# Kernel optimization log

Hardware: AMD Instinct MI355X
Metric: run time of the kernel (lower is better)

The kernel has to match this reference:

```python
import jax, jax.numpy as jnp
import numpy as np

M = 4  # mixture size of the AttentionStem value embedding

def unfold_windows(a, kh, kw, Hout, Wout):
    # a: [..., Hp, Wp] -> [..., Hout, Wout, kh, kw] (stride-1 sliding windows, cropped)
    rows = []
    for i in range(kh):
        cols = [a[..., i:i + Hout, j:j + Wout] for j in range(kw)]
        rows.append(jnp.stack(cols, axis=-1))
    return jnp.stack(rows, axis=-2)

def attention_stem(x, qw, kw_, vw, emb_a, emb_b, emb_mix, kh, kw, pad):
    # x: [B,Cin,H,W]; qw/kw_: [Cin,Co]; vw: [M,Cin,Co]; emb_a:[Co,kh]; emb_b:[Co,kw]; emb_mix:[M,Co]
    B, Cin, H, W = x.shape
    pl, pr, pt, pb = pad  # F.pad order (left,right,top,bottom)
    xp = jnp.pad(x, ((0, 0), (0, 0), (pt, pb), (pl, pr)))
    Hp, Wp = xp.shape[2], xp.shape[3]
    Hout = min(Hp - kh + 1, H)
    Wout = min(Wp - kw + 1, W)
    q = jnp.einsum('bchw,co->bohw', x[:, :, :Hout, :Wout], qw)       # 1x1 conv query
    k = jnp.einsum('bchw,co->bohw', xp, kw_)                          # 1x1 conv key on padded
    v = jnp.einsum('bchw,mco->mbohw', xp, vw)                         # m 1x1 conv values
    k_win = unfold_windows(k, kh, kw, Hout, Wout)                     # [B,Co,Ho,Wo,kh,kw]
    v_win = unfold_windows(v, kh, kw, Hout, Wout)                     # [M,B,Co,Ho,Wo,kh,kw]
    # mixture relative-position embedding, softmax over mixtures per (kh,kw) offset
    la = emb_mix @ emb_a                                              # [M,kh]
    lb = emb_mix @ emb_b                                              # [M,kw]
    emb = jax.nn.softmax(la[:, :, None] + lb[:, None, :], axis=0)     # [M,kh,kw]
    v_agg = jnp.einsum('mkl,mbohwkl->bohwkl', emb, v_win)             # [B,Co,Ho,Wo,kh,kw]
    K = kh * kw
    scores = jnp.einsum('bohw,bohwkl->bhwkl', q, k_win).reshape(B, Hout, Wout, K)
    attn = jax.nn.softmax(scores, axis=-1).reshape(B, Hout, Wout, kh, kw)
    out = jnp.einsum('bhwkl,bohwkl->bohw', attn, v_agg)               # [B,Co,Ho,Wo]
    return out

def bn_relu(x, g, b):
    # training-mode BatchNorm2d + ReLU
    mu = x.mean(axis=(0, 2, 3), keepdims=True)
    var = x.var(axis=(0, 2, 3), keepdims=True)
    y = (x - mu) * jax.lax.rsqrt(var + 1e-5) * g[None, :, None, None] + b[None, :, None, None]
    return jax.nn.relu(y)

def _params(key):
    ks = jax.random.split(key, 18)
    def w(k, shape):
        return jax.random.normal(k, shape, dtype=jnp.float32) * 0.1
    cfg = [(1, 64, 1, 5), (64, 128, 2, 5), (128, 16, 2, 5)]
    p = {}
    i = 0
    for s, (ci, co, kh, kw) in enumerate(cfg):
        p[f'p{s}_q'] = w(ks[i], (ci, co)); i += 1
        p[f'p{s}_k'] = w(ks[i], (ci, co)); i += 1
        p[f'p{s}_v'] = w(ks[i], (M, ci, co)); i += 1
        p[f'p{s}_ea'] = w(ks[i], (co, kh)); i += 1
        p[f'p{s}_eb'] = w(ks[i], (co, kw)); i += 1
        p[f'p{s}_em'] = w(ks[i], (M, co)); i += 1
        p[f'p{s}_g'] = jnp.ones((co,), jnp.float32)
        p[f'p{s}_b'] = jnp.zeros((co,), jnp.float32)
    return p

def setup_inputs() -> dict:
    key = jax.random.key(0)
    kx, kp = jax.random.split(key)
    inp = {'x': jax.random.normal(kx, (2, 1, 8, 3000), dtype=jnp.float32)}
    inp.update(_params(kp))
    return inp

def reference(x,
              p0_q, p0_k, p0_v, p0_ea, p0_eb, p0_em, p0_g, p0_b,
              p1_q, p1_k, p1_v, p1_ea, p1_eb, p1_em, p1_g, p1_b,
              p2_q, p2_k, p2_v, p2_ea, p2_eb, p2_em, p2_g, p2_b):
    h = attention_stem(x, p0_q, p0_k, p0_v, p0_ea, p0_eb, p0_em, 1, 5, (2, 2, 0, 0))
    h = bn_relu(h, p0_g, p0_b)[:, :, ::2, ::2]                        # MaxPool2d(1,2) == stride-2 subsample
    h = attention_stem(h, p1_q, p1_k, p1_v, p1_ea, p1_eb, p1_em, 2, 5, (2, 2, 1, 1))
    h = bn_relu(h, p1_g, p1_b)[:, :, ::2, ::2]
    h = attention_stem(h, p2_q, p2_k, p2_v, p2_ea, p2_eb, p2_em, 2, 5, (2, 2, 0, 0))
    h = bn_relu(h, p2_g, p2_b)
    B, C, H, W = h.shape
    nW = W // 56                                                       # AvgPool2d((1,56))
    return h[:, :, :, :nW * 56].reshape(B, C, H, nW, 56).mean(-1)
```

## Files before the change

kernel.cpp:

```cpp
#include <hip/hip_runtime.h>
#include <math.h>


#define TPB 256

__global__ void prep0_kernel(const float* __restrict__ ea,
                             const float* __restrict__ eb,
                             const float* __restrict__ em,
                             const float* __restrict__ qw,
                             const float* __restrict__ kw_,
                             const float* __restrict__ vw,
                             float* __restrict__ par) {
    const int M4 = 4, Co = 64, kw = 5;
    __shared__ float la[4];
    __shared__ float lb[20];
    __shared__ float embs[20];
    int tid = threadIdx.x;
    if (tid < 64) {
        float p = qw[tid] * kw_[tid];
#pragma unroll
        for (int d = 1; d < 64; d <<= 1) p += __shfl_xor(p, d, 64);
        if (tid == 0) par[0] = p;
    }
    if (tid >= 64 && tid < 64 + M4) {
        int m = tid - 64;
        float s = 0.f;
        for (int o = 0; o < Co; ++o) s += em[m * Co + o] * ea[o];
        la[m] = s;
    }
    if (tid >= 128 && tid < 128 + M4 * kw) {
        int r = tid - 128;
        int m = r / kw, l = r % kw;
        float s = 0.f;
        for (int o = 0; o < Co; ++o) s += em[m * Co + o] * eb[o * kw + l];
        lb[m * kw + l] = s;
    }
    __syncthreads();
    if (tid < 5) {
        float lg[4];
        float mx = -1e30f;
        for (int m = 0; m < M4; ++m) {
            lg[m] = la[m] + lb[m * kw + tid];
            mx = fmaxf(mx, lg[m]);
        }
        float sum = 0.f;
        for (int m = 0; m < M4; ++m) { lg[m] = expf(lg[m] - mx); sum += lg[m]; }
        float inv = 1.f / sum;
        for (int m = 0; m < M4; ++m) embs[tid * 4 + m] = lg[m] * inv;
    }
    __syncthreads();
    for (int e = tid; e < 5 * 64; e += blockDim.x) {
        int t = e / 64, o = e - t * 64;
        float s = 0.f;
        for (int m = 0; m < M4; ++m) s += embs[t * 4 + m] * vw[m * 64 + o];
        par[1 + e] = s;
    }
}

__global__ void attn_out0_kernel(const float* __restrict__ x,
                                 const float* __restrict__ par,
                                 float* __restrict__ h0raw,
                                 float2* __restrict__ part0) {
    __shared__ float wsh[5][256];
    __shared__ float vsh[5 * 64];
    __shared__ float wred[4][20];
    __shared__ float wfin[20];
    int tid = threadIdx.x;
    int b = blockIdx.y;
    int oz = blockIdx.z;
    int n0 = blockIdx.x * 256;
    int n = n0 + tid;
    for (int i = tid; i < 320; i += 256) vsh[i] = par[1 + i];
    float c0 = par[0];
    float warr[5];
    if (n < 24000) {
        int h = n / 3000, w = n - h * 3000;
        const float* xr = x + b * 24000 + h * 3000;
        float xc = xr[w];
        float xs[5], s[5];
#pragma unroll
        for (int t = 0; t < 5; ++t) {
            int col = w + t - 2;
            xs[t] = (col >= 0 && col < 3000) ? xr[col] : 0.f;
            s[t] = c0 * xc * xs[t];
        }
        float mx = s[0];
#pragma unroll
        for (int t = 1; t < 5; ++t) mx = fmaxf(mx, s[t]);
        float sum = 0.f;
#pragma unroll
        for (int t = 0; t < 5; ++t) { s[t] = expf(s[t] - mx); sum += s[t]; }
        float inv = 1.f / sum;
#pragma unroll
        for (int t = 0; t < 5; ++t) warr[t] = s[t] * inv * xs[t];
    } else {
#pragma unroll
        for (int t = 0; t < 5; ++t) warr[t] = 0.f;
    }
#pragma unroll
    for (int t = 0; t < 5; ++t) wsh[t][tid] = warr[t];
    float p[20];
#pragma unroll
    for (int t = 0; t < 5; ++t) p[t] = warr[t];
    {
        int k = 5;
#pragma unroll
        for (int t = 0; t < 5; ++t)
#pragma unroll
            for (int t2 = t; t2 < 5; ++t2) p[k++] = warr[t] * warr[t2];
    }
#pragma unroll
    for (int d = 1; d < 64; d <<= 1)
#pragma unroll
        for (int i = 0; i < 20; ++i) p[i] += __shfl_xor(p[i], d, 64);
    if ((tid & 63) == 0)
#pragma unroll
        for (int i = 0; i < 20; ++i) wred[tid >> 6][i] = p[i];
    __syncthreads();
    if (tid < 20)
        wfin[tid] = wred[0][tid] + wred[1][tid] + wred[2][tid] + wred[3][tid];
    __syncthreads();
    int jq = tid & 63, og = tid >> 6;
    int nq = n0 + jq * 4;
    int h = nq / 3000, w0 = nq - h * 3000;
    bool st = (nq < 24000) && ((h & 1) == 0);
    float wq[5][4];
#pragma unroll
    for (int t = 0; t < 5; ++t)
#pragma unroll
        for (int j = 0; j < 4; ++j) wq[t][j] = wsh[t][jq * 4 + j];
    int obase = oz * 32 + og * 8;
    for (int oi = 0; oi < 8; ++oi) {
        int o = obase + oi;
        float4 v = make_float4(0.f, 0.f, 0.f, 0.f);
#pragma unroll
        for (int t = 0; t < 5; ++t) {
            float vo = vsh[t * 64 + o];
            v.x = fmaf(wq[t][0], vo, v.x);
            v.y = fmaf(wq[t][1], vo, v.y);
            v.z = fmaf(wq[t][2], vo, v.z);
            v.w = fmaf(wq[t][3], vo, v.w);
        }
        if (st) {
            size_t base = ((size_t)b * 64 + o) * 6000 + (h >> 1) * 1500 + (w0 >> 1);
            *(float2*)&h0raw[base] = make_float2(v.x, v.z);
        }
    }
    if (tid < 32) {
        int o = oz * 32 + tid;
        float vt[5];
#pragma unroll
        for (int t = 0; t < 5; ++t) vt[t] = vsh[t * 64 + o];
        float s = 0.f, s2 = 0.f;
#pragma unroll
        for (int t = 0; t < 5; ++t) s = fmaf(vt[t], wfin[t], s);
        int k = 5;
#pragma unroll
        for (int t = 0; t < 5; ++t)
#pragma unroll
            for (int t2 = t; t2 < 5; ++t2) {
                float coef = (t == t2) ? vt[t] * vt[t] : 2.f * vt[t] * vt[t2];
                s2 = fmaf(coef, wfin[k], s2);
                ++k;
            }
        int chunk = b * gridDim.x + blockIdx.x;
        part0[(size_t)o * 188 + chunk] = make_float2(s, s2);
    }
}

__global__ void prep_stage1_kernel(const float* __restrict__ ea,
                                   const float* __restrict__ eb,
                                   const float* __restrict__ em,
                                   const float* __restrict__ qw,
                                   const float* __restrict__ kw_,
                                   const float* __restrict__ vw,
                                   float* __restrict__ Wqk,
                                   float* __restrict__ Av,
                                   const float2* __restrict__ part0,
                                   float* __restrict__ mr0) {
    const int M4 = 4, Co = 128, kh = 2, kw = 5, Cin = 64;
    __shared__ float la[8];
    __shared__ float lb[20];
    __shared__ float embs[40];
    int tid = threadIdx.x;
    if (blockIdx.x == 0 && tid < 64) {
        double s = 0.0, s2 = 0.0;
        for (int i = 0; i < 188; ++i) {
            float2 p = part0[(size_t)tid * 188 + i];
            s += p.x; s2 += p.y;
        }
        double mean = s / 48000.0;
        double var = s2 / 48000.0 - mean * mean;
        mr0[tid] = (float)mean;
        mr0[64 + tid] = (float)(1.0 / sqrt(var + 1e-5));
    }
    if (tid < M4 * kh) {
        int m = tid / kh, k = tid % kh;
        float s = 0.f;
        for (int o = 0; o < Co; ++o) s += em[m * Co + o] * ea[o * kh + k];
        la[tid] = s;
    }
    if (tid >= 64 && tid < 64 + M4 * kw) {
        int r = tid - 64;
        int m = r / kw, l = r % kw;
        float s = 0.f;
        for (int o = 0; o < Co; ++o) s += em[m * Co + o] * eb[o * kw + l];
        lb[r] = s;
    }
    __syncthreads();
    if (tid < 10) {
        int k = tid / kw, l = tid % kw;
        float lg[4];
        float mx = -1e30f;
        for (int m = 0; m < M4; ++m) {
            lg[m] = la[m * kh + k] + lb[m * kw + l];
            mx = fmaxf(mx, lg[m]);
        }
        float sum = 0.f;
        for (int m = 0; m < M4; ++m) { lg[m] = expf(lg[m] - mx); sum += lg[m]; }
        float inv = 1.f / sum;
        for (int m = 0; m < M4; ++m) embs[tid * 4 + m] = lg[m] * inv;
    }
    __syncthreads();
    const int TOT1 = 256 * 64;
    const int TOT2 = 640 * 128;
    for (int e = blockIdx.x * blockDim.x + tid; e < TOT1 + TOT2;
         e += gridDim.x * blockDim.x) {
        if (e < TOT1) {
            int m = e / Cin, c = e - m * Cin;
            Wqk[e] = (m < Co) ? qw[c * Co + m] : kw_[c * Co + (m - Co)];
        } else {
            int e2 = e - TOT1;
            int k = e2 / Co, o = e2 - k * Co;
            int c = k / 10, t = k - c * 10;
            float val = 0.f;
            for (int m = 0; m < M4; ++m)
                val += embs[t * 4 + m] * vw[(m * Cin + c) * Co + o];
            Av[e2] = val;
        }
    }
}

__global__ void prep_wcat_kernel(const float* __restrict__ ea,
                                 const float* __restrict__ eb,
                                 const float* __restrict__ em,
                                 const float* __restrict__ qw,
                                 const float* __restrict__ kw_,
                                 const float* __restrict__ vw,
                                 float* __restrict__ Wcat,
                                 int Co, int kh, int kw, int Cin,
                                 const float2* __restrict__ part,
                                 float* __restrict__ mr,
                                 int Cprev, int NCH, int count) {
    const int M4 = 4;
    __shared__ float la[8];
    __shared__ float lb[20];
    __shared__ float embs[40];
    int K = kh * kw;
    int tid = threadIdx.x;
    if (blockIdx.x == 0 && tid < Cprev) {
        double s = 0.0, s2 = 0.0;
        for (int i = 0; i < NCH; ++i) {
            float2 p = part[(size_t)tid * NCH + i];
            s += p.x; s2 += p.y;
        }
        double mean = s / count;
        double var = s2 / count - mean * mean;
        mr[tid] = (float)mean;
        mr[Cprev + tid] = (float)(1.0 / sqrt(var + 1e-5));
    }
    if (tid < M4 * kh) {
        int m = tid / kh, k = tid % kh;
        float s = 0.f;
        for (int o = 0; o < Co; ++o) s += em[m * Co + o] * ea[o * kh + k];
        la[tid] = s;
    }
    if (tid >= 64 && tid < 64 + M4 * kw) {
        int r = tid - 64;
        int m = r / kw, l = r % kw;
        float s = 0.f;
        for (int o = 0; o < Co; ++o) s += em[m * Co + o] * eb[o * kw + l];
        lb[r] = s;
    }
    __syncthreads();
    if (tid < K) {
        int k = tid / kw, l = tid % kw;
        float lg[4];
        float mx = -1e30f;
        for (int m = 0; m < M4; ++m) {
            lg[m] = la[m * kh + k] + lb[m * kw + l];
            mx = fmaxf(mx, lg[m]);
        }
        float sum = 0.f;
        for (int m = 0; m < M4; ++m) { lg[m] = expf(lg[m] - mx); sum += lg[m]; }
        float inv = 1.f / sum;
        for (int m = 0; m < M4; ++m) embs[tid * 4 + m] = lg[m] * inv;
    }
    __syncthreads();
    int Mtot = (2 + K) * Co;
    long long total = (long long)Mtot * Cin;
    for (long long e = (long long)blockIdx.x * blockDim.x + tid; e < total;
         e += (long long)gridDim.x * blockDim.x) {
        int m = (int)(e / Cin);
        int c = (int)(e - (long long)m * Cin);
        float val;
        if (m < Co) {
            val = qw[c * Co + m];
        } else if (m < 2 * Co) {
            val = kw_[c * Co + (m - Co)];
        } else {
            int mz = m - 2 * Co;
            int t = mz / Co;
            int o = mz - t * Co;
            val = 0.f;
            for (int mm = 0; mm < M4; ++mm)
                val += embs[t * 4 + mm] * vw[(mm * Cin + c) * Co + o];
        }
        Wcat[e] = val;
    }
}

__launch_bounds__(256, 4)
__global__ void gemm_qkbn_kernel(const float* __restrict__ A,
                                 const float* __restrict__ xraw,
                                 const float* __restrict__ mr,
                                 const float* __restrict__ g,
                                 const float* __restrict__ bb,
                                 float* __restrict__ qk,
                                 float* __restrict__ z,
                                 int M, int N, int K, int twoCo) {
    __shared__ float As[32][132];
    __shared__ float Bs[32][132];
    __shared__ float scale[128], shift[128];
    int tid = threadIdx.x;
    int b = blockIdx.z;
    int m0 = blockIdx.y * 128, n0 = blockIdx.x * 128;
    int Mz = M - twoCo;
    float acc[8][8] = {{0.f}};
    int am = tid >> 1, ak = (tid & 1) * 16;
    int bk = tid >> 3, bn = (tid & 7) * 16;
    int tm = tid & 15, tn = tid >> 4;
    for (int c = tid; c < K; c += 256) {
        float sc = mr[K + c] * g[c];
        scale[c] = sc;
        shift[c] = bb[c] - mr[c] * sc;
    }
    __syncthreads();

    for (int k0 = 0; k0 < K; k0 += 32) {
        {
            int mA = m0 + am;
            const float* Ap = A + (size_t)mA * K + k0 + ak;
#pragma unroll
            for (int q = 0; q < 4; ++q) {
                float4 v = (mA < M) ? *(const float4*)(Ap + q * 4)
                                    : make_float4(0.f, 0.f, 0.f, 0.f);
                int kk = ak + q * 4;
                As[kk + 0][am] = v.x;
                As[kk + 1][am] = v.y;
                As[kk + 2][am] = v.z;
                As[kk + 3][am] = v.w;
            }
        }
        {
            int c = k0 + bk;
            float sc = scale[c], sf = shift[c];
            const float* Xp = xraw + ((size_t)b * K + c) * N + n0 + bn;
            if (n0 + 128 <= N) {
#pragma unroll
                for (int q = 0; q < 4; ++q) {
                    float4 v = *(const float4*)(Xp + q * 4);
                    v.x = fmaxf(fmaf(v.x, sc, sf), 0.f);
                    v.y = fmaxf(fmaf(v.y, sc, sf), 0.f);
                    v.z = fmaxf(fmaf(v.z, sc, sf), 0.f);
                    v.w = fmaxf(fmaf(v.w, sc, sf), 0.f);
                    *(float4*)&Bs[bk][bn + q * 4] = v;
                }
            } else {
#pragma unroll
                for (int q = 0; q < 16; ++q) {
                    int n = n0 + bn + q;
                    Bs[bk][bn + q] = (n < N) ? fmaxf(fmaf(Xp[q], sc, sf), 0.f) : 0.f;
                }
            }
        }
        __syncthreads();
#pragma unroll 8
        for (int k = 0; k < 32; ++k) {
            float4 a0 = *(const float4*)&As[k][tm * 4];
            float4 a1 = *(const float4*)&As[k][64 + tm * 4];
            float4 b0 = *(const float4*)&Bs[k][tn * 4];
            float4 b1 = *(const float4*)&Bs[k][64 + tn * 4];
            float av[8] = {a0.x, a0.y, a0.z, a0.w, a1.x, a1.y, a1.z, a1.w};
            float bv[8] = {b0.x, b0.y, b0.z, b0.w, b1.x, b1.y, b1.z, b1.w};
#pragma unroll
            for (int i = 0; i < 8; ++i)
#pragma unroll
                for (int j = 0; j < 8; ++j)
                    acc[i][j] = fmaf(av[i], bv[j], acc[i][j]);
        }
        __syncthreads();
    }
    bool fullN = (n0 + 128 <= N);
#pragma unroll
    for (int iq = 0; iq < 2; ++iq) {
        int mb = m0 + iq * 64 + tm * 4;
        if (mb >= M) continue;
        if (mb < twoCo) {
#pragma unroll
            for (int jq = 0; jq < 2; ++jq)
#pragma unroll
                for (int jj = 0; jj < 4; ++jj) {
                    int n = n0 + jq * 64 + tn * 4 + jj;
                    if (n < N) {
                        float4 v = make_float4(acc[iq * 4 + 0][jq * 4 + jj],
                                               acc[iq * 4 + 1][jq * 4 + jj],
                                               acc[iq * 4 + 2][jq * 4 + jj],
                                               acc[iq * 4 + 3][jq * 4 + jj]);
                        *(float4*)&qk[((size_t)b * N + n) * twoCo + mb] = v;
                    }
                }
        } else {
#pragma unroll
            for (int i = 0; i < 4; ++i) {
                int row = mb + i - twoCo;
                float* zp = &z[((size_t)b * Mz + row) * N];
#pragma unroll
                for (int jq = 0; jq < 2; ++jq) {
                    int nb_ = n0 + jq * 64 + tn * 4;
                    if (fullN) {
                        *(float4*)&zp[nb_] = make_float4(acc[iq * 4 + i][jq * 4 + 0],
                                                         acc[iq * 4 + i][jq * 4 + 1],
                                                         acc[iq * 4 + i][jq * 4 + 2],
                                                         acc[iq * 4 + i][jq * 4 + 3]);
                    } else {
#pragma unroll
                        for (int jj = 0; jj < 4; ++jj)
                            if (nb_ + jj < N) zp[nb_ + jj] = acc[iq * 4 + i][jq * 4 + jj];
                    }
                }
            }
        }
    }
}

template <int KH, int KW, int CO, int NPB>
__global__ void attn_v3_kernel(const float* __restrict__ qk,
                               float* __restrict__ attn,
                               int H, int W, int Ho, int Wo, int pt, int pl) {
    const int K = KH * KW;
    __shared__ float ssh[NPB][K];
    int tid = threadIdx.x;
    int b = blockIdx.y;
    int ln = tid / K, t = tid - ln * K;
    int Nout = Ho * Wo;
    int n = blockIdx.x * NPB + ln;
    bool active = (tid < NPB * K) && (n < Nout);
    int HWin = H * W;
    float sv = 0.f;
    if (active) {
        int ho = n / Wo, wo = n - ho * Wo;
        int row = ho + t / KW - pt, col = wo + t % KW - pl;
        if (row >= 0 && row < H && col >= 0 && col < W) {
            const float* qp = qk + ((size_t)b * HWin + ho * W + wo) * (2 * CO);
            const float* kp = qk + ((size_t)b * HWin + (size_t)row * W + col) * (2 * CO) + CO;
#pragma unroll
            for (int o = 0; o < CO; o += 4) {
                float4 q4 = *(const float4*)(qp + o);
                float4 k4 = *(const float4*)(kp + o);
                sv += q4.x * k4.x + q4.y * k4.y + q4.z * k4.z + q4.w * k4.w;
            }
        }
        ssh[ln][t] = sv;
    }
    __syncthreads();
    if (active) {
        float mx = ssh[ln][0];
#pragma unroll
        for (int tt = 1; tt < K; ++tt) mx = fmaxf(mx, ssh[ln][tt]);
        float sum = 0.f;
#pragma unroll
        for (int tt = 0; tt < K; ++tt) sum += expf(ssh[ln][tt] - mx);
        float num = expf(sv - mx);
        attn[((size_t)b * K + t) * Nout + n] = num / sum;
    }
}

template <int KH, int KW, int SK>
__launch_bounds__(256)
__global__ void vgemm_kernel(const float* __restrict__ Av,
                             const float* __restrict__ xraw,
                             const float* __restrict__ attn,
                             const float* __restrict__ mr,
                             const float* __restrict__ g,
                             const float* __restrict__ bb,
                             float* __restrict__ partial,
                             int Cin, int Co,
                             int H, int W, int Ho, int Wo,
                             int pt, int pl) {
    const int KK = KH * KW;
    const int BK = 4 * KK;
    __shared__ float As[BK][68];
    __shared__ float Bs[BK][68];
    __shared__ float scale[128], shift[128];
    __shared__ float attn_s[KK][64];
    __shared__ int ho_s[64], wo_s[64];
    int tid = threadIdx.x;
    int b = blockIdx.z;
    int mt = blockIdx.y / SK, sk = blockIdx.y % SK;
    int m0 = mt * 64;
    int n0 = blockIdx.x * 64;
    int Nin = H * W, Nout = Ho * Wo;
    int Cpb = Cin / SK;
    int c_base = sk * Cpb;
    int Klocal = Cpb * KK;
    for (int c = tid; c < Cin; c += 256) {
        float sc = mr[Cin + c] * g[c];
        scale[c] = sc;
        shift[c] = bb[c] - mr[c] * sc;
    }
    for (int e = tid; e < KK * 64; e += 256) {
        int t = e >> 6, j = e & 63;
        int n = n0 + j;
        attn_s[t][j] = (n < Nout) ? attn[((size_t)b * KK + t) * Nout + n] : 0.f;
    }
    if (tid < 64) {
        int n = n0 + tid;
        ho_s[tid] = n / Wo;
        wo_s[tid] = n % Wo;
    }
    __syncthreads();
    float acc[4][4] = {{0.f}};
    int tm = tid & 15, tn = tid >> 4;
    for (int k0 = 0; k0 < Klocal; k0 += BK) {
#pragma unroll
        for (int it = 0; it < 10; ++it) {
            int e = it * 256 + tid;
            int kk = e >> 6, mm = e & 63;
            As[kk][mm] = Av[(size_t)(c_base * KK + k0 + kk) * Co + m0 + mm];
        }
#pragma unroll
        for (int it = 0; it < 10; ++it) {
            int e = it * 256 + tid;
            int kk = e >> 6, j = e & 63;
            int kg = k0 + kk;
            int cc = c_base + kg / KK, t = kg % KK;
            int dk = t / KW, dl = t % KW;
            int row = ho_s[j] + dk - pt;
            int col = wo_s[j] + dl - pl;
            float v = 0.f;
            if ((n0 + j) < Nout && row >= 0 && row < H && col >= 0 && col < W) {
                float xv = xraw[((size_t)b * Cin + cc) * Nin + row * W + col];
                xv = fmaxf(fmaf(xv, scale[cc], shift[cc]), 0.f);
                v = xv * attn_s[t][j];
            }
            Bs[kk][j] = v;
        }
        __syncthreads();
#pragma unroll 8
        for (int k = 0; k < BK; ++k) {
            float4 a4 = *(const float4*)&As[k][tm * 4];
            float4 b4 = *(const float4*)&Bs[k][tn * 4];
            float av[4] = {a4.x, a4.y, a4.z, a4.w};
            float bv[4] = {b4.x, b4.y, b4.z, b4.w};
#pragma unroll
            for (int i = 0; i < 4; ++i)
#pragma unroll
                for (int j = 0; j < 4; ++j)
                    acc[i][j] = fmaf(av[i], bv[j], acc[i][j]);
        }
        __syncthreads();
    }
    int B = gridDim.z;
#pragma unroll
    for (int i = 0; i < 4; ++i) {
        int o = m0 + tm * 4 + i;
        float* pp = &partial[(((size_t)sk * B + b) * Co + o) * Nout];
        int n = n0 + tn * 4;
        if (n + 3 < Nout) {
            *(float4*)&pp[n] = make_float4(acc[i][0], acc[i][1], acc[i][2], acc[i][3]);
        } else {
#pragma unroll
            for (int j = 0; j < 4; ++j)
                if (n + j < Nout) pp[n + j] = acc[i][j];
        }
    }
}

__global__ void vreduce_kernel(const float* __restrict__ partial,
                               float* __restrict__ h1raw,
                               float2* __restrict__ part1) {
    int tid = threadIdx.x;
    int by = blockIdx.y;
    int b = by >> 7, o = by & 127;
    int n = blockIdx.x * 1024 + tid * 4;
    float4 v = make_float4(0.f, 0.f, 0.f, 0.f);
    if (n < 6000) {
#pragma unroll
        for (int sk = 0; sk < 4; ++sk) {
            float4 p = *(const float4*)&partial[(((size_t)sk * 2 + b) * 128 + o) * 6000 + n];
            v.x += p.x; v.y += p.y; v.z += p.z; v.w += p.w;
        }
        int ho = n / 1500, wo = n - ho * 1500;
        if ((ho & 1) == 0) {
            size_t base = ((size_t)b * 128 + o) * 1500 + (ho >> 1) * 750 + (wo >> 1);
            *(float2*)&h1raw[base] = make_float2(v.x, v.z);
        }
    }
    float s = v.x + v.y + v.z + v.w;
    float s2 = v.x * v.x + v.y * v.y + v.z * v.z + v.w * v.w;
    __shared__ float sh[TPB], sh2[TPB];
    sh[tid] = s; sh2[tid] = s2;
    __syncthreads();
    for (int st = TPB / 2; st > 0; st >>= 1) {
        if (tid < st) { sh[tid] += sh[tid + st]; sh2[tid] += sh2[tid + st]; }
        __syncthreads();
    }
    if (tid == 0)
        part1[(size_t)o * 12 + b * 6 + blockIdx.x] = make_float2(sh[0], sh2[0]);
}

template <int KH, int KW>
__global__ void combine_stats_kernel(const float* __restrict__ z,
                                     const float* __restrict__ attn,
                                     float* __restrict__ out,
                                     float2* __restrict__ part,
                                     int Co, int Mz,
                                     int H, int W, int Ho, int Wo,
                                     int pt, int pl) {
    const int K = KH * KW;
    int tid = threadIdx.x;
    int bc = blockIdx.y;
    int b = bc / Co, o = bc - b * Co;
    int Nout = Ho * Wo, Nin = H * W;
    int n = blockIdx.x * blockDim.x + tid;
    float val = 0.f;
    if (n < Nout) {
        int ho = n / Wo, wo = n - ho * Wo;
#pragma unroll
        for (int dk = 0; dk < KH; ++dk) {
            int row = ho + dk - pt;
            if (row < 0 || row >= H) continue;
#pragma unroll
            for (int dl = 0; dl < KW; ++dl) {
                int col = wo + dl - pl;
                if (col < 0 || col >= W) continue;
                int t = dk * KW + dl;
                float a = attn[((size_t)b * K + t) * Nout + n];
                float zv = z[((size_t)b * Mz + t * Co + o) * Nin + row * W + col];
                val = fmaf(a, zv, val);
            }
        }
        out[((size_t)b * Co + o) * Nout + n] = val;
    }
    __shared__ float sh[TPB], sh2[TPB];
    sh[tid] = (n < Nout) ? val : 0.f;
    sh2[tid] = (n < Nout) ? val * val : 0.f;
    __syncthreads();
    for (int st = TPB / 2; st > 0; st >>= 1) {
        if (tid < st) { sh[tid] += sh[tid + st]; sh2[tid] += sh2[tid + st]; }
        __syncthreads();
    }
    if (tid == 0) {
        int chunk = b * gridDim.x + blockIdx.x;
        part[(size_t)o * (2 * gridDim.x) + chunk] = make_float2(sh[0], sh2[0]);
    }
}

__global__ void bn_avg_final_kernel(const float* __restrict__ x,
                                    const float2* __restrict__ part,
                                    const float* __restrict__ g,
                                    const float* __restrict__ bb,
                                    float* __restrict__ out,
                                    int B, int C, int W, int nW, int NCH) {
    int idx = blockIdx.x * blockDim.x + threadIdx.x;
    int N = B * C * nW;
    if (idx >= N) return;
    int j = idx % nW; int r = idx / nW;
    int c = r % C; int b = r / C;
    double s = 0.0, s2 = 0.0;
    for (int i = 0; i < NCH; ++i) {
        float2 p = part[(size_t)c * NCH + i];
        s += p.x; s2 += p.y;
    }
    double cnt = (double)B * W;
    double mean = s / cnt;
    double var = s2 / cnt - mean * mean;
    float rstd = (float)(1.0 / sqrt(var + 1e-5));
    float meanf = (float)mean, gg = g[c], bo = bb[c];
    const float* xb = x + ((long long)b * C + c) * W + j * 56;
    float acc = 0.f;
    for (int i = 0; i < 56; ++i) {
        float yn = (xb[i] - meanf) * rstd * gg + bo;
        acc += fmaxf(yn, 0.f);
    }
    out[idx] = acc * (1.f / 56.f);
}

extern "C" void kernel_launch(void* const* d_in, const int* in_sizes, int n_in,
                              void* d_out, int out_size, void* d_ws, size_t ws_size,
                              hipStream_t stream) {
    const float* x   = (const float*)d_in[0];
    const float* qw0 = (const float*)d_in[1];
    const float* kw0 = (const float*)d_in[2];
    const float* vw0 = (const float*)d_in[3];
    const float* ea0 = (const float*)d_in[4];
    const float* eb0 = (const float*)d_in[5];
    const float* em0 = (const float*)d_in[6];
    const float* g0  = (const float*)d_in[7];
    const float* b0  = (const float*)d_in[8];
    const float* qw1 = (const float*)d_in[9];
    const float* kw1 = (const float*)d_in[10];
    const float* vw1 = (const float*)d_in[11];
    const float* ea1 = (const float*)d_in[12];
    const float* eb1 = (const float*)d_in[13];
    const float* em1 = (const float*)d_in[14];
    const float* g1  = (const float*)d_in[15];
    const float* b1  = (const float*)d_in[16];
    const float* qw2 = (const float*)d_in[17];
    const float* kw2 = (const float*)d_in[18];
    const float* vw2 = (const float*)d_in[19];
    const float* ea2 = (const float*)d_in[20];
    const float* eb2 = (const float*)d_in[21];
    const float* em2 = (const float*)d_in[22];
    const float* g2  = (const float*)d_in[23];
    const float* b2  = (const float*)d_in[24];
    float* outp = (float*)d_out;
    (void)ws_size; (void)in_sizes; (void)n_in; (void)out_size;

    float* ws = (float*)d_ws;
    size_t off = 0;
    auto alloc = [&](size_t n) { float* p = ws + off; off += (n + 63) & ~(size_t)63; return p; };

    float* par0   = alloc(321);
    float* part0  = alloc(64 * 188 * 2);
    float* mr0    = alloc(128);
    float* h0raw  = alloc(2 * 64 * 6000);
    float* Wqk1   = alloc(256 * 64);
    float* Av1    = alloc(640 * 128);
    float* qk1    = alloc(2 * 6000 * 256);
    float* attn1  = alloc(2 * 10 * 6000);
    float* vpart  = alloc(4 * 2 * 128 * 6000);
    float* part1  = alloc(128 * 12 * 2);
    float* mr1    = alloc(256);
    float* h1raw  = alloc(2 * 128 * 1500);
    float* Wcat2  = alloc(192 * 128);
    float* qk2    = alloc(2 * 1500 * 32);
    float* z2     = alloc(2 * 160 * 1500);
    float* attn2  = alloc(2 * 10 * 750);
    float* part2  = alloc(16 * 6 * 2);
    float* s2     = alloc(2 * 16 * 750);

    auto grid = [](int n) { return (n + TPB - 1) / TPB; };

    prep0_kernel<<<1, TPB, 0, stream>>>(ea0, eb0, em0, qw0, kw0, vw0, par0);
    {
        dim3 g(94, 2, 2);
        attn_out0_kernel<<<g, TPB, 0, stream>>>(x, par0, h0raw, (float2*)part0);
    }
    prep_stage1_kernel<<<64, TPB, 0, stream>>>(ea1, eb1, em1, qw1, kw1, vw1,
        Wqk1, Av1, (const float2*)part0, mr0);
    {
        dim3 g(47, 2, 2);
        gemm_qkbn_kernel<<<g, TPB, 0, stream>>>(Wqk1, h0raw, mr0, g0, b0,
            qk1, qk1 , 256, 6000, 64, 256);
    }
    {
        dim3 g(6000 / 25, 2);
        attn_v3_kernel<2, 5, 128, 25><<<g, TPB, 0, stream>>>(qk1, attn1,
            4, 1500, 4, 1500, 1, 2);
    }
    {
        dim3 g(94, 2 * 4, 2);
        vgemm_kernel<2, 5, 4><<<g, TPB, 0, stream>>>(Av1, h0raw, attn1, mr0, g0, b0,
            vpart, 64, 128, 4, 1500, 4, 1500, 1, 2);
    }
    {
        dim3 g(6, 256);
        vreduce_kernel<<<g, TPB, 0, stream>>>(vpart, h1raw, (float2*)part1);
    }
    prep_wcat_kernel<<<24, TPB, 0, stream>>>(ea2, eb2, em2, qw2, kw2, vw2, Wcat2,
        16, 2, 5, 128, (const float2*)part1, mr1, 128, 12, 12000);
    {
        dim3 g(12, 2, 2);
        gemm_qkbn_kernel<<<g, TPB, 0, stream>>>(Wcat2, h1raw, mr1, g1, b1,
            qk2, z2, 192, 1500, 128, 32);
    }
    {
        dim3 g(750 / 25, 2);
        attn_v3_kernel<2, 5, 16, 25><<<g, TPB, 0, stream>>>(qk2, attn2,
            2, 750, 1, 750, 0, 2);
    }
    {
        dim3 g(3, 2 * 16);
        combine_stats_kernel<2, 5><<<g, TPB, 0, stream>>>(z2, attn2, s2,
            (float2*)part2, 16, 160, 2, 750, 1, 750, 0, 2);
    }
    bn_avg_final_kernel<<<grid(2 * 16 * 13), TPB, 0, stream>>>(s2, (const float2*)part2,
        g2, b2, outp, 2, 16, 750, 13, 6);
}
```

Measured before the change: 263.1 us.

## Fold q·k into Gram matrix and fuse stage-1 scores with softmax

Stage-1 attention scores are computed directly as x^T (Wq Wk^T) x using a precomputed 64x64 Gram matrix. This replaces the separate q/k GEMM that wrote a large qk buffer and the attention softmax pass, so both now run in one tiled kernel with a shared input window. The value GEMM is specialised to fixed shapes, stages the BN-ReLU input window and attention weights in shared memory, and halves the split-K factor, which shrinks the partial buffer and the reduction. In exchange each block does more serial work and the code is hardcoded to this layer's dimensions.

```diff
diff --git a/kernel.cpp b/kernel.cpp
--- a/kernel.cpp
+++ b/kernel.cpp
@@ -174,7 +174,7 @@
                                    const float* __restrict__ qw,
                                    const float* __restrict__ kw_,
                                    const float* __restrict__ vw,
-                                   float* __restrict__ Wqk,
+                                   float* __restrict__ G,
                                    float* __restrict__ Av,
                                    const float2* __restrict__ part0,
                                    float* __restrict__ mr0) {
@@ -222,15 +222,18 @@
         for (int m = 0; m < M4; ++m) embs[tid * 4 + m] = lg[m] * inv;
     }
     __syncthreads();
-    const int TOT1 = 256 * 64;
+    const int TOTG = 64 * 64;
     const int TOT2 = 640 * 128;
-    for (int e = blockIdx.x * blockDim.x + tid; e < TOT1 + TOT2;
-         e += gridDim.x * blockDim.x) {
-        if (e < TOT1) {
-            int m = e / Cin, c = e - m * Cin;
-            Wqk[e] = (m < Co) ? qw[c * Co + m] : kw_[c * Co + (m - Co)];
+    int nth = gridDim.x * blockDim.x;
+    for (int e = blockIdx.x * blockDim.x + tid; e < TOTG + TOT2; e += nth) {
+        if (e < TOTG) {
+            int c = e >> 6, c2 = e & 63;
+            float s = 0.f;
+            for (int o = 0; o < 128; ++o)
+                s = fmaf(qw[c * 128 + o], kw_[c2 * 128 + o], s);
+            G[e] = s;
         } else {
-            int e2 = e - TOT1;
+            int e2 = e - TOTG;
             int k = e2 / Co, o = e2 - k * Co;
             int c = k / 10, t = k - c * 10;
             float val = 0.f;
@@ -320,6 +323,216 @@
     }
 }
 
+__global__ void attn_v4_kernel(const float* __restrict__ G,
+                               const float* __restrict__ xraw,
+                               const float* __restrict__ mr,
+                               const float* __restrict__ g,
+                               const float* __restrict__ bb,
+                               float* __restrict__ attn) {
+    __shared__ float xw[64][2][68];
+    __shared__ float gbuf[64][64];
+    __shared__ float ssh[64][12];
+    __shared__ float scb[64], sfb[64];
+    int tid = threadIdx.x;
+    int chunk = blockIdx.x;
+    int ho = blockIdx.y;
+    int b = blockIdx.z;
+    int wo0 = chunk * 64;
+    if (tid < 64) {
+        float sc = mr[64 + tid] * g[tid];
+        scb[tid] = sc;
+        sfb[tid] = bb[tid] - mr[tid] * sc;
+    }
+    for (int e = tid; e < 4096; e += 256)
+        gbuf[e >> 6][e & 63] = G[e];
+    __syncthreads();
+    for (int e = tid; e < 64 * 136; e += 256) {
+        int c = e / 136;
+        int r2 = e - c * 136;
+        int r = r2 / 68, jj = r2 - r * 68;
+        int row = ho - 1 + r;
+        int col = wo0 + jj - 2;
+        float v = 0.f;
+        if (row >= 0 && col >= 0 && col < 1500) {
+            float xv = xraw[((size_t)b * 64 + c) * 6000 + row * 1500 + col];
+            v = fmaxf(fmaf(xv, scb[c], sfb[c]), 0.f);
+        }
+        xw[c][r][jj] = v;
+    }
+    __syncthreads();
+    int j = tid & 63, cg = tid >> 6;
+    float ul[16];
+#pragma unroll
+    for (int i = 0; i < 16; ++i) ul[i] = 0.f;
+    for (int c = 0; c < 64; ++c) {
+        float xv = xw[c][1][j + 2];
+#pragma unroll
+        for (int i = 0; i < 16; ++i)
+            ul[i] = fmaf(gbuf[c][cg * 16 + i], xv, ul[i]);
+    }
+    __syncthreads();
+#pragma unroll
+    for (int i = 0; i < 16; ++i) gbuf[cg * 16 + i][j] = ul[i];
+    __syncthreads();
+    int t0 = cg, t1 = cg + 4, t2 = cg + 8;
+    int dk0 = t0 / 5, dl0 = t0 % 5;
+    int dk1 = t1 / 5, dl1 = t1 % 5;
+    int dk2 = (t2 < 10) ? 1 : 0, dl2 = (t2 < 10) ? (t2 - 5) : 0;
+    float s0 = 0.f, s1 = 0.f, s2v = 0.f;
+    for (int c = 0; c < 64; ++c) {
+        float uv = gbuf[c][j];
+        s0 = fmaf(uv, xw[c][dk0][j + dl0], s0);
+        s1 = fmaf(uv, xw[c][dk1][j + dl1], s1);
+        if (t2 < 10) s2v = fmaf(uv, xw[c][dk2][j + dl2], s2v);
+    }
+    ssh[j][t0] = s0;
+    ssh[j][t1] = s1;
+    if (t2 < 10) ssh[j][t2] = s2v;
+    __syncthreads();
+    if (tid < 64 && wo0 + tid < 1500) {
+        float sc[10];
+        float mx = -1e30f;
+#pragma unroll
+        for (int t = 0; t < 10; ++t) { sc[t] = ssh[tid][t]; mx = fmaxf(mx, sc[t]); }
+        float sum = 0.f;
+#pragma unroll
+        for (int t = 0; t < 10; ++t) { sc[t] = expf(sc[t] - mx); sum += sc[t]; }
+        float inv = 1.f / sum;
+        int n = ho * 1500 + wo0 + tid;
+#pragma unroll
+        for (int t = 0; t < 10; ++t)
+            attn[((size_t)b * 10 + t) * 6000 + n] = sc[t] * inv;
+    }
+}
+
+__launch_bounds__(256)
+__global__ void vgemm_kernel(const float* __restrict__ Av,
+                             const float* __restrict__ xraw,
+                             const float* __restrict__ attn,
+                             const float* __restrict__ mr,
+                             const float* __restrict__ g,
+                             const float* __restrict__ bb,
+                             float* __restrict__ partial) {
+    __shared__ float As[40][68];
+    __shared__ float Bs[40][68];
+    __shared__ float xw[32][2][68];
+    __shared__ float att_s[10][64];
+    __shared__ float scl[32], sfl[32];
+    int tid = threadIdx.x;
+    int nt = blockIdx.x;
+    int ho = nt / 24, chunk = nt - ho * 24;
+    int wo0 = chunk * 64;
+    int my = blockIdx.y;
+    int mt = my >> 1, sk = my & 1;
+    int m0 = mt * 64;
+    int b = blockIdx.z;
+    int c_base = sk * 32;
+    if (tid < 32) {
+        int c = c_base + tid;
+        float sc = mr[64 + c] * g[c];
+        scl[tid] = sc;
+        sfl[tid] = bb[c] - mr[c] * sc;
+    }
+    __syncthreads();
+    for (int e = tid; e < 32 * 136; e += 256) {
+        int c = e / 136;
+        int r2 = e - c * 136;
+        int r = r2 / 68, jj = r2 - r * 68;
+        int row = ho - 1 + r;
+        int col = wo0 + jj - 2;
+        float v = 0.f;
+        if (row >= 0 && col >= 0 && col < 1500) {
+            float xv = xraw[((size_t)b * 64 + c_base + c) * 6000 + row * 1500 + col];
+            v = fmaxf(fmaf(xv, scl[c], sfl[c]), 0.f);
+        }
+        xw[c][r][jj] = v;
+    }
+    for (int e = tid; e < 640; e += 256) {
+        int t = e >> 6, jj = e & 63;
+        int col = wo0 + jj;
+        att_s[t][jj] = (col < 1500)
+            ? attn[((size_t)b * 10 + t) * 6000 + ho * 1500 + col] : 0.f;
+    }
+    __syncthreads();
+    float acc[4][4] = {{0.f}};
+    int tm = tid & 15, tn = tid >> 4;
+    int arow = c_base * 10;
+    for (int k0 = 0; k0 < 320; k0 += 40) {
+#pragma unroll
+        for (int it = 0; it < 10; ++it) {
+            int e = it * 256 + tid;
+            int kk = e >> 6, mm = e & 63;
+            As[kk][mm] = Av[(size_t)(arow + k0 + kk) * 128 + m0 + mm];
+        }
+#pragma unroll
+        for (int it = 0; it < 10; ++it) {
+            int e = it * 256 + tid;
+            int kk = e >> 6, jj = e & 63;
+            int kg = k0 + kk;
+            int cl = kg / 10, t = kg - cl * 10;
+            int dk = t / 5, dl = t - dk * 5;
+            Bs[kk][jj] = xw[cl][dk][jj + dl] * att_s[t][jj];
+        }
+        __syncthreads();
+#pragma unroll 8
+        for (int k = 0; k < 40; ++k) {
+            float4 a4 = *(const float4*)&As[k][tm * 4];
+            float4 b4 = *(const float4*)&Bs[k][tn * 4];
+            float av[4] = {a4.x, a4.y, a4.z, a4.w};
+            float bv[4] = {b4.x, b4.y, b4.z, b4.w};
+#pragma unroll
+            for (int i = 0; i < 4; ++i)
+#pragma unroll
+                for (int jx = 0; jx < 4; ++jx)
+                    acc[i][jx] = fmaf(av[i], bv[jx], acc[i][jx]);
+        }
+        __syncthreads();
+    }
+    int wo = wo0 + tn * 4;
+    if (wo < 1500) {
+        int n = ho * 1500 + wo;
+#pragma unroll
+        for (int i = 0; i < 4; ++i) {
+            int o = m0 + tm * 4 + i;
+            float* pp = &partial[(((size_t)sk * 2 + b) * 128 + o) * 6000 + n];
+            *(float4*)pp = make_float4(acc[i][0], acc[i][1], acc[i][2], acc[i][3]);
+        }
+    }
+}
+
+__global__ void vreduce_kernel(const float* __restrict__ partial,
+                               float* __restrict__ h1raw,
+                               float2* __restrict__ part1) {
+    int tid = threadIdx.x;
+    int by = blockIdx.y;
+    int b = by >> 7, o = by & 127;
+    int n = blockIdx.x * 1024 + tid * 4;
+    float4 v = make_float4(0.f, 0.f, 0.f, 0.f);
+    if (n < 6000) {
+#pragma unroll
+        for (int sk = 0; sk < 2; ++sk) {
+            float4 p = *(const float4*)&partial[(((size_t)sk * 2 + b) * 128 + o) * 6000 + n];
+            v.x += p.x; v.y += p.y; v.z += p.z; v.w += p.w;
+        }
+        int ho = n / 1500, wo = n - ho * 1500;
+        if ((ho & 1) == 0) {
+            size_t base = ((size_t)b * 128 + o) * 1500 + (ho >> 1) * 750 + (wo >> 1);
+            *(float2*)&h1raw[base] = make_float2(v.x, v.z);
+        }
+    }
+    float s = v.x + v.y + v.z + v.w;
+    float s2 = v.x * v.x + v.y * v.y + v.z * v.z + v.w * v.w;
+    __shared__ float sh[TPB], sh2[TPB];
+    sh[tid] = s; sh2[tid] = s2;
+    __syncthreads();
+    for (int st = TPB / 2; st > 0; st >>= 1) {
+        if (tid < st) { sh[tid] += sh[tid + st]; sh2[tid] += sh2[tid + st]; }
+        __syncthreads();
+    }
+    if (tid == 0)
+        part1[(size_t)o * 12 + b * 6 + blockIdx.x] = make_float2(sh[0], sh2[0]);
+}
+
 __launch_bounds__(256, 4)
 __global__ void gemm_qkbn_kernel(const float* __restrict__ A,
                                  const float* __restrict__ xraw,
@@ -346,7 +559,6 @@
         shift[c] = bb[c] - mr[c] * sc;
     }
     __syncthreads();
-
     for (int k0 = 0; k0 < K; k0 += 32) {
         {
             int mA = m0 + am;
@@ -484,140 +696,6 @@
         float num = expf(sv - mx);
         attn[((size_t)b * K + t) * Nout + n] = num / sum;
     }
-}
-
-template <int KH, int KW, int SK>
-__launch_bounds__(256)
-__global__ void vgemm_kernel(const float* __restrict__ Av,
-                             const float* __restrict__ xraw,
-                             const float* __restrict__ attn,
-                             const float* __restrict__ mr,
-                             const float* __restrict__ g,
-                             const float* __restrict__ bb,
-                             float* __restrict__ partial,
-                             int Cin, int Co,
-                             int H, int W, int Ho, int Wo,
-                             int pt, int pl) {
-    const int KK = KH * KW;
-    const int BK = 4 * KK;
-    __shared__ float As[BK][68];
-    __shared__ float Bs[BK][68];
-    __shared__ float scale[128], shift[128];
-    __shared__ float attn_s[KK][64];
-    __shared__ int ho_s[64], wo_s[64];
-    int tid = threadIdx.x;
-    int b = blockIdx.z;
-    int mt = blockIdx.y / SK, sk = blockIdx.y % SK;
-    int m0 = mt * 64;
-    int n0 = blockIdx.x * 64;
-    int Nin = H * W, Nout = Ho * Wo;
-    int Cpb = Cin / SK;
-    int c_base = sk * Cpb;
-    int Klocal = Cpb * KK;
-    for (int c = tid; c < Cin; c += 256) {
-        float sc = mr[Cin + c] * g[c];
-        scale[c] = sc;
-        shift[c] = bb[c] - mr[c] * sc;
-    }
-    for (int e = tid; e < KK * 64; e += 256) {
-        int t = e >> 6, j = e & 63;
-        int n = n0 + j;
-        attn_s[t][j] = (n < Nout) ? attn[((size_t)b * KK + t) * Nout + n] : 0.f;
-    }
-    if (tid < 64) {
-        int n = n0 + tid;
-        ho_s[tid] = n / Wo;
-        wo_s[tid] = n % Wo;
-    }
-    __syncthreads();
-    float acc[4][4] = {{0.f}};
-    int tm = tid & 15, tn = tid >> 4;
-    for (int k0 = 0; k0 < Klocal; k0 += BK) {
-#pragma unroll
-        for (int it = 0; it < 10; ++it) {
-            int e = it * 256 + tid;
-            int kk = e >> 6, mm = e & 63;
-            As[kk][mm] = Av[(size_t)(c_base * KK + k0 + kk) * Co + m0 + mm];
-        }
-#pragma unroll
-        for (int it = 0; it < 10; ++it) {
-            int e = it * 256 + tid;
-            int kk = e >> 6, j = e & 63;
-            int kg = k0 + kk;
-            int cc = c_base + kg / KK, t = kg % KK;
-            int dk = t / KW, dl = t % KW;
-            int row = ho_s[j] + dk - pt;
-            int col = wo_s[j] + dl - pl;
-            float v = 0.f;
-            if ((n0 + j) < Nout && row >= 0 && row < H && col >= 0 && col < W) {
-                float xv = xraw[((size_t)b * Cin + cc) * Nin + row * W + col];
-                xv = fmaxf(fmaf(xv, scale[cc], shift[cc]), 0.f);
-                v = xv * attn_s[t][j];
-            }
-            Bs[kk][j] = v;
-        }
-        __syncthreads();
-#pragma unroll 8
-        for (int k = 0; k < BK; ++k) {
-            float4 a4 = *(const float4*)&As[k][tm * 4];
-            float4 b4 = *(const float4*)&Bs[k][tn * 4];
-            float av[4] = {a4.x, a4.y, a4.z, a4.w};
-            float bv[4] = {b4.x, b4.y, b4.z, b4.w};
-#pragma unroll
-            for (int i = 0; i < 4; ++i)
-#pragma unroll
-                for (int j = 0; j < 4; ++j)
-                    acc[i][j] = fmaf(av[i], bv[j], acc[i][j]);
-        }
-        __syncthreads();
-    }
-    int B = gridDim.z;
-#pragma unroll
-    for (int i = 0; i < 4; ++i) {
-        int o = m0 + tm * 4 + i;
-        float* pp = &partial[(((size_t)sk * B + b) * Co + o) * Nout];
-        int n = n0 + tn * 4;
-        if (n + 3 < Nout) {
-            *(float4*)&pp[n] = make_float4(acc[i][0], acc[i][1], acc[i][2], acc[i][3]);
-        } else {
-#pragma unroll
-            for (int j = 0; j < 4; ++j)
-                if (n + j < Nout) pp[n + j] = acc[i][j];
-        }
-    }
-}
-
-__global__ void vreduce_kernel(const float* __restrict__ partial,
-                               float* __restrict__ h1raw,
-                               float2* __restrict__ part1) {
-    int tid = threadIdx.x;
-    int by = blockIdx.y;
-    int b = by >> 7, o = by & 127;
-    int n = blockIdx.x * 1024 + tid * 4;
-    float4 v = make_float4(0.f, 0.f, 0.f, 0.f);
-    if (n < 6000) {
-#pragma unroll
-        for (int sk = 0; sk < 4; ++sk) {
-            float4 p = *(const float4*)&partial[(((size_t)sk * 2 + b) * 128 + o) * 6000 + n];
-            v.x += p.x; v.y += p.y; v.z += p.z; v.w += p.w;
-        }
-        int ho = n / 1500, wo = n - ho * 1500;
-        if ((ho & 1) == 0) {
-            size_t base = ((size_t)b * 128 + o) * 1500 + (ho >> 1) * 750 + (wo >> 1);
-            *(float2*)&h1raw[base] = make_float2(v.x, v.z);
-        }
-    }
-    float s = v.x + v.y + v.z + v.w;
-    float s2 = v.x * v.x + v.y * v.y + v.z * v.z + v.w * v.w;
-    __shared__ float sh[TPB], sh2[TPB];
-    sh[tid] = s; sh2[tid] = s2;
-    __syncthreads();
-    for (int st = TPB / 2; st > 0; st >>= 1) {
-        if (tid < st) { sh[tid] += sh[tid + st]; sh2[tid] += sh2[tid + st]; }
-        __syncthreads();
-    }
-    if (tid == 0)
-        part1[(size_t)o * 12 + b * 6 + blockIdx.x] = make_float2(sh[0], sh2[0]);
 }
 
 template <int KH, int KW>
@@ -736,11 +814,10 @@
     float* part0  = alloc(64 * 188 * 2);
     float* mr0    = alloc(128);
     float* h0raw  = alloc(2 * 64 * 6000);
-    float* Wqk1   = alloc(256 * 64);
+    float* G1     = alloc(64 * 64);
     float* Av1    = alloc(640 * 128);
-    float* qk1    = alloc(2 * 6000 * 256);
     float* attn1  = alloc(2 * 10 * 6000);
-    float* vpart  = alloc(4 * 2 * 128 * 6000);
+    float* vpart  = alloc(2 * 2 * 128 * 6000);
     float* part1  = alloc(128 * 12 * 2);
     float* mr1    = alloc(256);
     float* h1raw  = alloc(2 * 128 * 1500);
@@ -759,21 +836,14 @@
         attn_out0_kernel<<<g, TPB, 0, stream>>>(x, par0, h0raw, (float2*)part0);
     }
     prep_stage1_kernel<<<64, TPB, 0, stream>>>(ea1, eb1, em1, qw1, kw1, vw1,
-        Wqk1, Av1, (const float2*)part0, mr0);
+        G1, Av1, (const float2*)part0, mr0);
     {
-        dim3 g(47, 2, 2);
-        gemm_qkbn_kernel<<<g, TPB, 0, stream>>>(Wqk1, h0raw, mr0, g0, b0,
-            qk1, qk1 , 256, 6000, 64, 256);
+        dim3 g(24, 4, 2);
+        attn_v4_kernel<<<g, TPB, 0, stream>>>(G1, h0raw, mr0, g0, b0, attn1);
     }
     {
-        dim3 g(6000 / 25, 2);
-        attn_v3_kernel<2, 5, 128, 25><<<g, TPB, 0, stream>>>(qk1, attn1,
-            4, 1500, 4, 1500, 1, 2);
-    }
-    {
-        dim3 g(94, 2 * 4, 2);
-        vgemm_kernel<2, 5, 4><<<g, TPB, 0, stream>>>(Av1, h0raw, attn1, mr0, g0, b0,
-            vpart, 64, 128, 4, 1500, 4, 1500, 1, 2);
+        dim3 g(96, 4, 2);
+        vgemm_kernel<<<g, TPB, 0, stream>>>(Av1, h0raw, attn1, mr0, g0, b0, vpart);
     }
     {
         dim3 g(6, 256);
```

New measurement: 259.2 us. About the same (-1.5%).
